# Kernel optimization log

Measured on AMD Instinct MI355X. Metric: run time of the kernel, lower is better.

## Reference

```python
import jax, jax.numpy as jnp
import numpy as np

DIM = 128

def _dwconv(x, w, b, pad):
    # x: [N,C,H,W], w: [C,1,kh,kw] depthwise (feature_group_count=C)
    y = jax.lax.conv_general_dilated(
        x, w, window_strides=(1, 1), padding=pad,
        dimension_numbers=('NCHW', 'OIHW', 'NCHW'),
        feature_group_count=x.shape[1])
    return y + b[None, :, None, None]

def setup_inputs() -> dict:
    key = jax.random.key(0)
    ks = jax.random.split(key, 13)
    d = DIM
    s = lambda k, shape, fan: jax.random.normal(k, shape, jnp.float32) * (1.0 / np.sqrt(fan))
    return {
        'x': jax.random.normal(ks[0], (16, d, 128, 128), jnp.float32),
        'w0':   s(ks[1], (d, 1, 3, 3), 9),   'b0':   jnp.zeros((d,), jnp.float32),
        'w0_1': s(ks[2], (d, 1, 1, 5), 5),   'b0_1': jnp.zeros((d,), jnp.float32),
        'w0_2': s(ks[3], (d, 1, 5, 1), 5),   'b0_2': jnp.zeros((d,), jnp.float32),
        'w1_1': s(ks[4], (d, 1, 1, 11), 11), 'b1_1': jnp.zeros((d,), jnp.float32),
        'w1_2': s(ks[5], (d, 1, 11, 1), 11), 'b1_2': jnp.zeros((d,), jnp.float32),
        'w3':   s(ks[6], (d, d, 1, 1), d),   'b3':   jnp.zeros((d,), jnp.float32),
    }

def reference(x, w0, b0, w0_1, b0_1, w0_2, b0_2, w1_1, b1_1, w1_2, b1_2, w3, b3):
    x_33  = _dwconv(x, w0, b0, ((1, 1), (1, 1)))
    x_15  = _dwconv(_dwconv(x, w0_1, b0_1, ((0, 0), (2, 2))), w0_2, b0_2, ((2, 2), (0, 0)))
    x_111 = _dwconv(_dwconv(x, w1_1, b1_1, ((0, 0), (5, 5))), w1_2, b1_2, ((5, 5), (0, 0)))
    add = x_33 + x_15 + x_111
    # 1x1 pointwise conv == channel mixing einsum
    mixer = jnp.einsum('nchw,oc->nohw', add, w3[:, :, 0, 0]) + b3[None, :, None, None]
    return mixer * x
```

## Files before the change

kernel.cpp:

```cpp
#include <hip/hip_runtime.h>
#include <stdint.h>

using f4v = __attribute__((ext_vector_type(4))) float;
using s8v = __attribute__((ext_vector_type(8))) short;

constexpr int C_ = 128, H_ = 128, W_ = 128, HW_ = H_ * W_;
constexpr int S_ = 4;
constexpr int OROWS = H_ / S_;
constexpr int CHB = 4;
constexpr int TPB = 512;
static_assert(OROWS == 32, "bias table indexing assumes 32 rows/block");

__device__ __forceinline__ unsigned f2bf(float f) {
  union { float f; unsigned u; } v; v.f = f;
  return (v.u + 0x7FFFu + ((v.u >> 16) & 1u)) >> 16;
}

__device__ __forceinline__ float sgpr(float v) {
  return __int_as_float(__builtin_amdgcn_readfirstlane(__float_as_int(v)));
}

__global__ __launch_bounds__(TPB) void k_dw(
    const float* __restrict__ x,
    const float* __restrict__ w0,  const float* __restrict__ b0,
    const float* __restrict__ w01, const float* __restrict__ b01,
    const float* __restrict__ w02, const float* __restrict__ b02,
    const float* __restrict__ w11, const float* __restrict__ b11,
    const float* __restrict__ w12, const float* __restrict__ b12,
    unsigned short* __restrict__ ws)
{
  __shared__ float xs[CHB][16][144];
  __shared__ unsigned short ebuf[16][CHB][128];
  __shared__ float bias_row[CHB][OROWS];

  const int t = threadIdx.x;
  const int yb = blockIdx.x, g = blockIdx.y, n = blockIdx.z;
  const int ch = t >> 7, xl = t & 127;
  const int c0 = g * CHB, c = c0 + ch;

  const int obase = yb * OROWS;
  const int oend  = obase + OROWS;
  const int sbase = (obase >= 5) ? (obase - 5) : 0;
  const int lastrow = (oend + 4 <= H_ - 1) ? (oend + 4) : (H_ - 1);
  const int nrows = lastrow - sbase + 1;
  const int nchunk = (nrows + 15) >> 4;

  float w0t[9], w01t[5], w02t[5], w11t[11], w12t[11];
#pragma unroll
  for (int k = 0; k < 9; ++k)  w0t[k] = sgpr(w0[c * 9 + k]);
#pragma unroll
  for (int k = 0; k < 5; ++k)  { w01t[k] = sgpr(w01[c * 5 + k]); w02t[k] = sgpr(w02[c * 5 + k]); }
#pragma unroll
  for (int k = 0; k < 11; ++k) { w11t[k] = sgpr(w11[c * 11 + k]); w12t[k] = sgpr(w12[c * 11 + k]); }

  if (t < CHB * OROWS) {
    const int cb = t >> 5, oo = t & 31;
    const int y = obase + oo, cc = c0 + cb;
    float s5 = 0.f, s11 = 0.f;
#pragma unroll
    for (int k = 0; k < 5; ++k)  if ((unsigned)(y - 2 + k) < 128u) s5  += w02[cc * 5 + k];
#pragma unroll
    for (int k = 0; k < 11; ++k) if ((unsigned)(y - 5 + k) < 128u) s11 += w12[cc * 11 + k];
    bias_row[cb][oo] = b0[cc] + b02[cc] + b12[cc] + b01[cc] * s5 + b11[cc] * s11;
  }

  if (t < 256) {
    const int zc = t >> 6, zr = (t >> 2) & 15, zq = t & 3;
    const int col = (zq < 2) ? zq * 4 : 136 + (zq - 2) * 4;
    *(float4*)&xs[zc][zr][col] = make_float4(0.f, 0.f, 0.f, 0.f);
  }

  float acc[16];
#pragma unroll
  for (int i = 0; i < 16; ++i) acc[i] = 0.f;

  unsigned short* wsp = ws + (size_t)(n * 32 + g) * HW_ * 4;

  for (int cidx = 0; cidx < nchunk; ++cidx) {
    const int r0g = sbase + cidx * 16;
    const int rem_rows = nrows - cidx * 16;
    const int rlim = rem_rows < 16 ? rem_rows : 16;
    __syncthreads();
#pragma unroll
    for (int i = 0; i < 4; ++i) {
      const int id = i * TPB + t;
      const int chs = id >> 9;
      const int rs  = (id >> 5) & 15;
      const int c4  = id & 31;
      float4 v = make_float4(0.f, 0.f, 0.f, 0.f);
      if (rs < rlim)
        v = *(const float4*)(x + (size_t)((n * C_ + c0 + chs) * H_ + r0g + rs) * W_ + c4 * 4);
      *(float4*)&xs[chs][rs][8 + c4 * 4] = v;
    }
    __syncthreads();
#pragma unroll
    for (int rr = 0; rr < 16; ++rr) {
      if (rr < rlim) {
        float win[11];
#pragma unroll
        for (int k = 0; k < 11; ++k) win[k] = xs[ch][rr][xl + 3 + k];
        float h11 = w11t[0] * win[0];
#pragma unroll
        for (int k = 1; k < 11; ++k) h11 += w11t[k] * win[k];
        float h5 = w01t[0] * win[3];
#pragma unroll
        for (int k = 1; k < 5; ++k) h5 += w01t[k] * win[3 + k];
        float r0v = w0t[0] * win[4] + w0t[1] * win[5] + w0t[2] * win[6];
        float r1v = w0t[3] * win[4] + w0t[4] * win[5] + w0t[5] * win[6];
        float r2v = w0t[6] * win[4] + w0t[7] * win[5] + w0t[8] * win[6];
#pragma unroll
        for (int tt = 0; tt < 11; ++tt) acc[(rr + 5 - tt) & 15] += w12t[tt] * h11;
#pragma unroll
        for (int tt = 0; tt < 5; ++tt)  acc[(rr + 2 - tt) & 15] += w02t[tt] * h5;
        acc[(rr + 1) & 15]  += r0v;
        acc[rr & 15]        += r1v;
        acc[(rr + 15) & 15] += r2v;
        const int o_e = r0g + rr - 5;
        const int slot = (rr + 11) & 15;
        if (o_e >= obase)
          ebuf[rr][ch][xl] = (unsigned short)f2bf(acc[slot] + bias_row[ch][o_e - obase]);
        acc[slot] = 0.f;
      }
    }
    __syncthreads();
    for (int id = t; id < 2048; id += TPB) {
      const int orr = id >> 7, px = id & 127;
      const int o = r0g + orr - 5;
      if (orr < rlim && o >= obase) {
        uint2 pk;
        pk.x = ebuf[orr][0][px] | ((unsigned)ebuf[orr][1][px] << 16);
        pk.y = ebuf[orr][2][px] | ((unsigned)ebuf[orr][3][px] << 16);
        *(uint2*)(wsp + ((size_t)o * W_ + px) * 4) = pk;
      }
    }
  }
  if (oend == H_) {
    __syncthreads();
#pragma unroll
    for (int orr = 0; orr < 5; ++orr) {
      const int o = H_ - 5 + orr;
      const int slot = (o - sbase) & 15;
      ebuf[orr][ch][xl] = (unsigned short)f2bf(acc[slot] + bias_row[ch][o - obase]);
    }
    __syncthreads();
    for (int id = t; id < 640; id += TPB) {
      const int orr = id >> 7, px = id & 127;
      const int o = H_ - 5 + orr;
      uint2 pk;
      pk.x = ebuf[orr][0][px] | ((unsigned)ebuf[orr][1][px] << 16);
      pk.y = ebuf[orr][2][px] | ((unsigned)ebuf[orr][3][px] << 16);
      *(uint2*)(wsp + ((size_t)o * W_ + px) * 4) = pk;
    }
  }
}

constexpr int PXB = 64;

__global__ __launch_bounds__(256) void k_mix(
    const float* __restrict__ x,
    const float* __restrict__ w3, const float* __restrict__ b3,
    const unsigned short* __restrict__ ws,
    float* __restrict__ out)
{
  const int t = threadIdx.x;
  const int wv = t >> 6, lane = t & 63, q = lane >> 4, lp = lane & 15;
  const int n = blockIdx.y;
  const int px0 = blockIdx.x * PXB;

  s8v A[2][4];
  float b3v[2][4];
#pragma unroll
  for (int m = 0; m < 2; ++m) {
    const int o = 32 * wv + 16 * m + lp;
#pragma unroll
    for (int ks = 0; ks < 4; ++ks) {
      const float* src = w3 + o * 128 + ks * 32 + q * 8;
      float4 f0 = *(const float4*)src;
      float4 f1 = *(const float4*)(src + 4);
      union { s8v v; unsigned u[4]; } pk;
      pk.u[0] = f2bf(f0.x) | (f2bf(f0.y) << 16);
      pk.u[1] = f2bf(f0.z) | (f2bf(f0.w) << 16);
      pk.u[2] = f2bf(f1.x) | (f2bf(f1.y) << 16);
      pk.u[3] = f2bf(f1.z) | (f2bf(f1.w) << 16);
      A[m][ks] = pk.v;
    }
#pragma unroll
    for (int r = 0; r < 4; ++r) b3v[m][r] = b3[32 * wv + 16 * m + 4 * q + r];
  }

  const unsigned short* wsn = ws + (size_t)n * 32 * HW_ * 4;

#pragma unroll
  for (int npg = 0; npg < PXB / 16; ++npg) {
    const int pp = px0 + npg * 16 + lp;
    s8v B[4];
#pragma unroll
    for (int ks = 0; ks < 4; ++ks) {
      const int gg8 = ks * 4 + q;
      const unsigned short* gsrc = wsn + ((size_t)(gg8 * 2) * HW_ + pp) * 4;
      union { s8v v; uint2 u2[2]; } pk;
      pk.u2[0] = *(const uint2*)gsrc;
      pk.u2[1] = *(const uint2*)(gsrc + (size_t)HW_ * 4);
      B[ks] = pk.v;
    }
    float xv[2][4];
#pragma unroll
    for (int m = 0; m < 2; ++m)
#pragma unroll
      for (int r = 0; r < 4; ++r) {
        const int o = 32 * wv + 16 * m + 4 * q + r;
        xv[m][r] = x[((size_t)(n * C_ + o) << 14) + pp];
      }
    f4v acc[2] = {{0.f,0.f,0.f,0.f},{0.f,0.f,0.f,0.f}};
#pragma unroll
    for (int ks = 0; ks < 4; ++ks) {
#pragma unroll
      for (int m = 0; m < 2; ++m)
        acc[m] = __builtin_amdgcn_mfma_f32_16x16x32_bf16(A[m][ks], B[ks], acc[m], 0, 0, 0);
    }
#pragma unroll
    for (int m = 0; m < 2; ++m)
#pragma unroll
      for (int r = 0; r < 4; ++r) {
        const int o = 32 * wv + 16 * m + 4 * q + r;
        const size_t idx = ((size_t)(n * C_ + o) << 14) + pp;
        out[idx] = (acc[m][r] + b3v[m][r]) * xv[m][r];
      }
  }
}

extern "C" void kernel_launch(void* const* d_in, const int* in_sizes, int n_in,
                              void* d_out, int out_size, void* d_ws, size_t ws_size,
                              hipStream_t stream) {
  const float* x   = (const float*)d_in[0];
  const float* w0  = (const float*)d_in[1];
  const float* b0  = (const float*)d_in[2];
  const float* w01 = (const float*)d_in[3];
  const float* b01 = (const float*)d_in[4];
  const float* w02 = (const float*)d_in[5];
  const float* b02 = (const float*)d_in[6];
  const float* w11 = (const float*)d_in[7];
  const float* b11 = (const float*)d_in[8];
  const float* w12 = (const float*)d_in[9];
  const float* b12 = (const float*)d_in[10];
  const float* w3  = (const float*)d_in[11];
  const float* b3  = (const float*)d_in[12];
  unsigned short* ws = (unsigned short*)d_ws;
  float* out = (float*)d_out;

  dim3 g1(S_, 32, 16);
  k_dw<<<g1, TPB, 0, stream>>>(x, w0, b0, w01, b01, w02, b02, w11, b11, w12, b12, ws);

  dim3 g2(HW_ / PXB, 16);
  k_mix<<<g2, 256, 0, stream>>>(x, w3, b3, ws, out);
}
```

Baseline: 362.3 us.

## Pipeline depthwise row staging in 8-row halves and transpose mix output via LDS

The depthwise kernel now processes 8-row chunks instead of 16. The next chunk's global load is issued alongside the bf16 writeout of the current one, which halves LDS use and overlaps load with store. A template parameter keeps the 16-entry accumulator ring indices compile-time constant across alternating halves. The mix kernel swaps the MFMA operands so results land channel-major in an LDS tile, then does vectorized float4 loads of x and stores of out with 512 threads per block, replacing scattered scalar accesses. The risks are extra LDS traffic and barriers in both kernels.

```diff
diff --git a/kernel.cpp b/kernel.cpp
--- a/kernel.cpp
+++ b/kernel.cpp
@@ -19,6 +19,8 @@
 __device__ __forceinline__ float sgpr(float v) {
   return __int_as_float(__builtin_amdgcn_readfirstlane(__float_as_int(v)));
 }
+
+template <int P> struct Par { static constexpr int v = P; };
 
 __global__ __launch_bounds__(TPB) void k_dw(
     const float* __restrict__ x,
@@ -29,8 +31,8 @@
     const float* __restrict__ w12, const float* __restrict__ b12,
     unsigned short* __restrict__ ws)
 {
-  __shared__ float xs[CHB][16][144];
-  __shared__ unsigned short ebuf[16][CHB][128];
+  __shared__ float xs[CHB][8][144];
+  __shared__ unsigned short ebuf[8][CHB][128];
   __shared__ float bias_row[CHB][OROWS];
 
   const int t = threadIdx.x;
@@ -43,7 +45,7 @@
   const int sbase = (obase >= 5) ? (obase - 5) : 0;
   const int lastrow = (oend + 4 <= H_ - 1) ? (oend + 4) : (H_ - 1);
   const int nrows = lastrow - sbase + 1;
-  const int nchunk = (nrows + 15) >> 4;
+  const int nhalf = (nrows + 7) >> 3;
 
   float w0t[9], w01t[5], w02t[5], w11t[11], w12t[11];
 #pragma unroll
@@ -64,8 +66,8 @@
     bias_row[cb][oo] = b0[cc] + b02[cc] + b12[cc] + b01[cc] * s5 + b11[cc] * s11;
   }
 
-  if (t < 256) {
-    const int zc = t >> 6, zr = (t >> 2) & 15, zq = t & 3;
+  if (t < 128) {
+    const int zc = t >> 5, zr = (t >> 2) & 7, zq = t & 3;
     const int col = (zq < 2) ? zq * 4 : 136 + (zq - 2) * 4;
     *(float4*)&xs[zc][zr][col] = make_float4(0.f, 0.f, 0.f, 0.f);
   }
@@ -76,66 +78,83 @@
 
   unsigned short* wsp = ws + (size_t)(n * 32 + g) * HW_ * 4;
 
-  for (int cidx = 0; cidx < nchunk; ++cidx) {
-    const int r0g = sbase + cidx * 16;
-    const int rem_rows = nrows - cidx * 16;
-    const int rlim = rem_rows < 16 ? rem_rows : 16;
-    __syncthreads();
-#pragma unroll
-    for (int i = 0; i < 4; ++i) {
+  auto stage = [&](int hh) {
+    const int rb = 8 * hh;
+#pragma unroll
+    for (int i = 0; i < 2; ++i) {
       const int id = i * TPB + t;
-      const int chs = id >> 9;
-      const int rs  = (id >> 5) & 15;
+      const int chs = id >> 8;
+      const int rs  = (id >> 5) & 7;
       const int c4  = id & 31;
       float4 v = make_float4(0.f, 0.f, 0.f, 0.f);
-      if (rs < rlim)
-        v = *(const float4*)(x + (size_t)((n * C_ + c0 + chs) * H_ + r0g + rs) * W_ + c4 * 4);
+      if (rb + rs < nrows)
+        v = *(const float4*)(x + (size_t)((n * C_ + c0 + chs) * H_ + sbase + rb + rs) * W_ + c4 * 4);
       *(float4*)&xs[chs][rs][8 + c4 * 4] = v;
     }
-    __syncthreads();
-#pragma unroll
-    for (int rr = 0; rr < 16; ++rr) {
-      if (rr < rlim) {
-        float win[11];
-#pragma unroll
-        for (int k = 0; k < 11; ++k) win[k] = xs[ch][rr][xl + 3 + k];
-        float h11 = w11t[0] * win[0];
-#pragma unroll
-        for (int k = 1; k < 11; ++k) h11 += w11t[k] * win[k];
-        float h5 = w01t[0] * win[3];
-#pragma unroll
-        for (int k = 1; k < 5; ++k) h5 += w01t[k] * win[3 + k];
-        float r0v = w0t[0] * win[4] + w0t[1] * win[5] + w0t[2] * win[6];
-        float r1v = w0t[3] * win[4] + w0t[4] * win[5] + w0t[5] * win[6];
-        float r2v = w0t[6] * win[4] + w0t[7] * win[5] + w0t[8] * win[6];
-#pragma unroll
-        for (int tt = 0; tt < 11; ++tt) acc[(rr + 5 - tt) & 15] += w12t[tt] * h11;
-#pragma unroll
-        for (int tt = 0; tt < 5; ++tt)  acc[(rr + 2 - tt) & 15] += w02t[tt] * h5;
-        acc[(rr + 1) & 15]  += r0v;
-        acc[rr & 15]        += r1v;
-        acc[(rr + 15) & 15] += r2v;
-        const int o_e = r0g + rr - 5;
-        const int slot = (rr + 11) & 15;
-        if (o_e >= obase)
-          ebuf[rr][ch][xl] = (unsigned short)f2bf(acc[slot] + bias_row[ch][o_e - obase]);
-        acc[slot] = 0.f;
-      }
-    }
-    __syncthreads();
-    for (int id = t; id < 2048; id += TPB) {
+  };
+
+  auto writeout = [&](int hh, int hl) {
+    const int rbg = sbase + 8 * hh;
+    for (int id = t; id < 1024; id += TPB) {
       const int orr = id >> 7, px = id & 127;
-      const int o = r0g + orr - 5;
-      if (orr < rlim && o >= obase) {
+      const int o = rbg + orr - 5;
+      if (orr < hl && o >= obase) {
         uint2 pk;
         pk.x = ebuf[orr][0][px] | ((unsigned)ebuf[orr][1][px] << 16);
         pk.y = ebuf[orr][2][px] | ((unsigned)ebuf[orr][3][px] << 16);
         *(uint2*)(wsp + ((size_t)o * W_ + px) * 4) = pk;
       }
     }
+  };
+
+  auto compute = [&](auto par, int hh, int hl) {
+    constexpr int PAR = decltype(par)::v;
+    const int rbg = sbase + 8 * hh;
+#pragma unroll
+    for (int rr = 0; rr < 8; ++rr) {
+      if (rr < hl) {
+        float win[11];
+#pragma unroll
+        for (int k = 0; k < 11; ++k) win[k] = xs[ch][rr][xl + 3 + k];
+        float h11 = w11t[0] * win[0];
+#pragma unroll
+        for (int k = 1; k < 11; ++k) h11 += w11t[k] * win[k];
+        float h5 = w01t[0] * win[3];
+#pragma unroll
+        for (int k = 1; k < 5; ++k) h5 += w01t[k] * win[3 + k];
+        float r0v = w0t[0] * win[4] + w0t[1] * win[5] + w0t[2] * win[6];
+        float r1v = w0t[3] * win[4] + w0t[4] * win[5] + w0t[5] * win[6];
+        float r2v = w0t[6] * win[4] + w0t[7] * win[5] + w0t[8] * win[6];
+        const int re = PAR + rr;
+#pragma unroll
+        for (int tt = 0; tt < 11; ++tt) acc[(re + 5 - tt) & 15] += w12t[tt] * h11;
+#pragma unroll
+        for (int tt = 0; tt < 5; ++tt)  acc[(re + 2 - tt) & 15] += w02t[tt] * h5;
+        acc[(re + 1) & 15]  += r0v;
+        acc[re & 15]        += r1v;
+        acc[(re + 15) & 15] += r2v;
+        const int o_e = rbg + rr - 5;
+        const int slot = (re + 11) & 15;
+        if (o_e >= obase)
+          ebuf[rr][ch][xl] = (unsigned short)f2bf(acc[slot] + bias_row[ch][o_e - obase]);
+        acc[slot] = 0.f;
+      }
+    }
+  };
+
+  stage(0);
+  __syncthreads();
+  for (int hh = 0; hh < nhalf; ++hh) {
+    const int rem = nrows - 8 * hh;
+    const int hl = rem < 8 ? rem : 8;
+    if (hh & 1) compute(Par<8>{}, hh, hl);
+    else        compute(Par<0>{}, hh, hl);
+    __syncthreads();
+    if (hh + 1 < nhalf) stage(hh + 1);
+    writeout(hh, hl);
+    __syncthreads();
   }
   if (oend == H_) {
-    __syncthreads();
 #pragma unroll
     for (int orr = 0; orr < 5; ++orr) {
       const int o = H_ - 5 + orr;
@@ -154,78 +173,75 @@
   }
 }
 
-constexpr int PXB = 64;
-
-__global__ __launch_bounds__(256) void k_mix(
+constexpr int MPX = 64;
+
+__global__ __launch_bounds__(512) void k_mix(
     const float* __restrict__ x,
     const float* __restrict__ w3, const float* __restrict__ b3,
     const unsigned short* __restrict__ ws,
     float* __restrict__ out)
 {
+  __shared__ float xp[128][66];
+
   const int t = threadIdx.x;
   const int wv = t >> 6, lane = t & 63, q = lane >> 4, lp = lane & 15;
   const int n = blockIdx.y;
-  const int px0 = blockIdx.x * PXB;
-
-  s8v A[2][4];
-  float b3v[2][4];
-#pragma unroll
-  for (int m = 0; m < 2; ++m) {
-    const int o = 32 * wv + 16 * m + lp;
+  const int pxb = blockIdx.x * MPX;
+  const int o0 = wv * 16;
+
+  s8v Bw[4];
+#pragma unroll
+  for (int ks = 0; ks < 4; ++ks) {
+    const float* src = w3 + (o0 + lp) * 128 + ks * 32 + q * 8;
+    float4 f0 = *(const float4*)src;
+    float4 f1 = *(const float4*)(src + 4);
+    union { s8v v; unsigned u[4]; } pk;
+    pk.u[0] = f2bf(f0.x) | (f2bf(f0.y) << 16);
+    pk.u[1] = f2bf(f0.z) | (f2bf(f0.w) << 16);
+    pk.u[2] = f2bf(f1.x) | (f2bf(f1.y) << 16);
+    pk.u[3] = f2bf(f1.z) | (f2bf(f1.w) << 16);
+    Bw[ks] = pk.v;
+  }
+
+  const unsigned short* wsn = ws + (size_t)n * 32 * HW_ * 4;
+
+#pragma unroll
+  for (int st = 0; st < 4; ++st) {
+    const int pp = pxb + st * 16 + lp;
+    s8v Aa[4];
 #pragma unroll
     for (int ks = 0; ks < 4; ++ks) {
-      const float* src = w3 + o * 128 + ks * 32 + q * 8;
-      float4 f0 = *(const float4*)src;
-      float4 f1 = *(const float4*)(src + 4);
-      union { s8v v; unsigned u[4]; } pk;
-      pk.u[0] = f2bf(f0.x) | (f2bf(f0.y) << 16);
-      pk.u[1] = f2bf(f0.z) | (f2bf(f0.w) << 16);
-      pk.u[2] = f2bf(f1.x) | (f2bf(f1.y) << 16);
-      pk.u[3] = f2bf(f1.z) | (f2bf(f1.w) << 16);
-      A[m][ks] = pk.v;
-    }
-#pragma unroll
-    for (int r = 0; r < 4; ++r) b3v[m][r] = b3[32 * wv + 16 * m + 4 * q + r];
-  }
-
-  const unsigned short* wsn = ws + (size_t)n * 32 * HW_ * 4;
-
-#pragma unroll
-  for (int npg = 0; npg < PXB / 16; ++npg) {
-    const int pp = px0 + npg * 16 + lp;
-    s8v B[4];
-#pragma unroll
-    for (int ks = 0; ks < 4; ++ks) {
-      const int gg8 = ks * 4 + q;
-      const unsigned short* gsrc = wsn + ((size_t)(gg8 * 2) * HW_ + pp) * 4;
+      const unsigned short* gsrc = wsn + ((size_t)(ks * 8 + 2 * q) * HW_ + pp) * 4;
       union { s8v v; uint2 u2[2]; } pk;
       pk.u2[0] = *(const uint2*)gsrc;
       pk.u2[1] = *(const uint2*)(gsrc + (size_t)HW_ * 4);
-      B[ks] = pk.v;
-    }
-    float xv[2][4];
-#pragma unroll
-    for (int m = 0; m < 2; ++m)
-#pragma unroll
-      for (int r = 0; r < 4; ++r) {
-        const int o = 32 * wv + 16 * m + 4 * q + r;
-        xv[m][r] = x[((size_t)(n * C_ + o) << 14) + pp];
-      }
-    f4v acc[2] = {{0.f,0.f,0.f,0.f},{0.f,0.f,0.f,0.f}};
-#pragma unroll
-    for (int ks = 0; ks < 4; ++ks) {
-#pragma unroll
-      for (int m = 0; m < 2; ++m)
-        acc[m] = __builtin_amdgcn_mfma_f32_16x16x32_bf16(A[m][ks], B[ks], acc[m], 0, 0, 0);
-    }
-#pragma unroll
-    for (int m = 0; m < 2; ++m)
-#pragma unroll
-      for (int r = 0; r < 4; ++r) {
-        const int o = 32 * wv + 16 * m + 4 * q + r;
-        const size_t idx = ((size_t)(n * C_ + o) << 14) + pp;
-        out[idx] = (acc[m][r] + b3v[m][r]) * xv[m][r];
-      }
+      Aa[ks] = pk.v;
+    }
+    f4v acc = {0.f, 0.f, 0.f, 0.f};
+#pragma unroll
+    for (int ks = 0; ks < 4; ++ks)
+      acc = __builtin_amdgcn_mfma_f32_16x16x32_bf16(Aa[ks], Bw[ks], acc, 0, 0, 0);
+    float2 lo; lo.x = acc[0]; lo.y = acc[1];
+    float2 hi; hi.x = acc[2]; hi.y = acc[3];
+    *(float2*)&xp[o0 + lp][st * 16 + 4 * q]     = lo;
+    *(float2*)&xp[o0 + lp][st * 16 + 4 * q + 2] = hi;
+  }
+  __syncthreads();
+
+#pragma unroll
+  for (int s = 0; s < 4; ++s) {
+    const int chv = s * 32 + wv * 4 + q;
+    const float b3c = b3[chv];
+    float2 p0 = *(const float2*)&xp[chv][lp * 4];
+    float2 p1 = *(const float2*)&xp[chv][lp * 4 + 2];
+    const size_t base = ((size_t)(n * C_ + chv) << 14) + pxb + lp * 4;
+    float4 xv = *(const float4*)(x + base);
+    float4 ov;
+    ov.x = (p0.x + b3c) * xv.x;
+    ov.y = (p0.y + b3c) * xv.y;
+    ov.z = (p1.x + b3c) * xv.z;
+    ov.w = (p1.y + b3c) * xv.w;
+    *(float4*)(out + base) = ov;
   }
 }
 
@@ -251,6 +267,6 @@
   dim3 g1(S_, 32, 16);
   k_dw<<<g1, TPB, 0, stream>>>(x, w0, b0, w01, b01, w02, b02, w11, b11, w12, b12, ws);
 
-  dim3 g2(HW_ / PXB, 16);
-  k_mix<<<g2, 256, 0, stream>>>(x, w3, b3, ws, out);
-}
+  dim3 g2(HW_ / MPX, 16);
+  k_mix<<<g2, 512, 0, stream>>>(x, w3, b3, ws, out);
+}
```

New measurement: 388.3 us. 7.2% more time.
